# Kernel tuning notes

Measured on AMD Instinct MI355X. Metric: run time of the kernel, lower is better.

Reference implementation:

```python
import jax, jax.numpy as jnp
import numpy as np

BATCH = 8192
VOCAB = 16384
EMBED = 256
EPS = 1e-6


def setup_inputs() -> dict:
    key = jax.random.key(0)
    k1, k2 = jax.random.split(key)
    # multi-hot indicator input: values in {0,1}; only nonzero positions matter
    x = jax.random.randint(k1, (BATCH, VOCAB), 0, 2, dtype=jnp.int32)
    # learned embedding table (nn.Embedding weight)
    emb = jax.random.normal(k2, (VOCAB, EMBED), dtype=jnp.float32)
    return {"x": x, "emb": emb}


def reference(x, emb):
    # torch: gather embeddings at nonzero (row, col) pairs, scatter-add per row,
    # divide by per-row nonzero count (+eps). Equivalent jit-friendly form:
    # mask @ emb gives the per-row sum of embeddings over nonzero columns.
    mask = (x != 0).astype(emb.dtype)               # [B, V]
    embed_sum = mask @ emb                           # [B, E]
    count = jnp.sum(mask, axis=1, keepdims=True) + EPS  # [B, 1]
    return embed_sum / count
```

## Files before the change

### kernel.cpp

```cpp
#include <hip/hip_runtime.h>
#include <hip/hip_bf16.h>
#include <stdint.h>

#define BATCH 8192
#define VOCAB 16384
#define EMBED 256

#define BM 64
#define BK 64
#define KSPLIT 4
#define KRANGE (VOCAB / KSPLIT)
#define KITERS (KRANGE / BK)
#define MTILES (BATCH / BM)

typedef __attribute__((ext_vector_type(4))) float    f32x4;
typedef __attribute__((ext_vector_type(4))) int      i32x4;
typedef __attribute__((ext_vector_type(4))) unsigned u32x4;

#define EMB_WS_BYTES ((size_t)VOCAB * EMBED * 2)

__device__ __forceinline__ void gload_lds16(const void* g, void* l) {
    __builtin_amdgcn_global_load_lds(
        (const __attribute__((address_space(1))) unsigned int*)(uintptr_t)g,
        (__attribute__((address_space(3))) unsigned int*)(uint32_t)(uintptr_t)l,
        16, 0, 0);
}

__device__ __forceinline__ void mfma_bf16(f32x4& acc, i32x4 a, i32x4 b) {
    asm("v_mfma_f32_16x16x32_bf16 %0, %1, %2, %0" : "+v"(acc) : "v"(a), "v"(b));
}

__global__ __launch_bounds__(256) void prep_kernel(
    const float* __restrict__ emb, unsigned short* __restrict__ emb_ws,
    float* __restrict__ out)
{
    int t = blockIdx.x * 256 + threadIdx.x;
    ((f32x4*)out)[t] = (f32x4){0.f, 0.f, 0.f, 0.f};

    int ko = t >> 8;
    int e  = t & 255;
    union { unsigned short s[8]; u32x4 q; } v;
    #pragma unroll
    for (int j = 0; j < 8; ++j) {
        float f = emb[(size_t)(ko * 8 + j) * EMBED + e];
        unsigned u = __float_as_uint(f);
        u += 0x7FFFu + ((u >> 16) & 1u);
        v.s[j] = (unsigned short)(u >> 16);
    }
    int kt  = ko >> 3;
    int kk0 = (ko & 7) * 8;
    unsigned byt = (unsigned)(e * 128 + ((kk0 * 2) ^ ((e & 7) << 4)));
    *(u32x4*)((char*)emb_ws + (size_t)kt * 32768 + byt) = v.q;
}

__global__ __launch_bounds__(256) void gemm_kernel(
    const int* __restrict__ x, const unsigned short* __restrict__ emb_ws,
    float* __restrict__ out, int* __restrict__ cnt_ws)
{
    __shared__ __align__(16) unsigned short As[BM * BK];
    __shared__ __align__(16) unsigned short Bs[EMBED * BK];

    int bid   = blockIdx.x;
    int mt    = bid & (MTILES - 1);
    int split = bid >> 7;

    int tid  = threadIdx.x;
    int lane = tid & 63;
    int wave = tid >> 6;

    int ar = tid >> 2;
    int aq = tid & 3;
    const int*  aptr  = x + (size_t)(mt * BM + ar) * VOCAB + split * KRANGE + aq * 4;
    const char* bbase = (const char*)emb_ws + (size_t)split * KITERS * 32768;

    int cnt = 0;
    f32x4 acc[4][4];
    #pragma unroll
    for (int i = 0; i < 4; ++i)
        #pragma unroll
        for (int j = 0; j < 4; ++j) acc[i][j] = (f32x4){0.f, 0.f, 0.f, 0.f};

    for (int kt = 0; kt < KITERS; ++kt) {
        const char* bsrc = bbase + (size_t)kt * 32768 + tid * 16;
        #pragma unroll
        for (int i = 0; i < 8; ++i)
            gload_lds16(bsrc + i * 4096, (char*)Bs + tid * 16 + i * 4096);

        const int* ap = aptr + kt * BK;
        i32x4 av[4];
        #pragma unroll
        for (int j = 0; j < 4; ++j) av[j] = *(const i32x4*)(ap + j * 16);

        #pragma unroll
        for (int j = 0; j < 4; ++j) {
            unsigned lo = (av[j].x ? 0x3F80u : 0u) | (av[j].y ? 0x3F800000u : 0u);
            unsigned hi = (av[j].z ? 0x3F80u : 0u) | (av[j].w ? 0x3F800000u : 0u);
            cnt += (av[j].x != 0) + (av[j].y != 0) + (av[j].z != 0) + (av[j].w != 0);
            int kk = aq * 4 + j * 16;
            unsigned byt = (unsigned)(ar * 128 + ((kk * 2) ^ ((ar & 7) << 4)));
            *(uint2*)((char*)As + byt) = make_uint2(lo, hi);
        }

        __syncthreads();

        #pragma unroll
        for (int ks = 0; ks < 2; ++ks) {
            int kg = ks * 32 + (lane >> 4) * 8;
            i32x4 af[4], bf[4];
            #pragma unroll
            for (int fm = 0; fm < 4; ++fm) {
                int row = fm * 16 + (lane & 15);
                af[fm] = *(const i32x4*)((const char*)As + row * 128 +
                                         ((kg * 2) ^ ((row & 7) << 4)));
            }
            #pragma unroll
            for (int fe = 0; fe < 4; ++fe) {
                int e = wave * 64 + fe * 16 + (lane & 15);
                bf[fe] = *(const i32x4*)((const char*)Bs + e * 128 +
                                         ((kg * 2) ^ ((e & 7) << 4)));
            }
            #pragma unroll
            for (int fm = 0; fm < 4; ++fm)
                #pragma unroll
                for (int fe = 0; fe < 4; ++fe)
                    mfma_bf16(acc[fm][fe], af[fm], bf[fe]);
        }
        __syncthreads();
    }

    cnt += __shfl_xor(cnt, 1);
    cnt += __shfl_xor(cnt, 2);
    if (aq == 0) cnt_ws[split * BATCH + mt * BM + ar] = cnt;

    #pragma unroll
    for (int fm = 0; fm < 4; ++fm)
        #pragma unroll
        for (int fe = 0; fe < 4; ++fe)
            asm volatile("s_nop 7\n\ts_nop 7" : "+v"(acc[fm][fe]));

    #pragma unroll
    for (int fm = 0; fm < 4; ++fm) {
        int row = mt * BM + fm * 16 + (lane >> 4) * 4;
        #pragma unroll
        for (int fe = 0; fe < 4; ++fe) {
            int col = wave * 64 + fe * 16 + (lane & 15);
            float* p = out + (size_t)row * EMBED + col;
            #pragma unroll
            for (int r = 0; r < 4; ++r)
                atomicAdd(p + (size_t)r * EMBED, acc[fm][fe][r]);
        }
    }
}

__global__ __launch_bounds__(256) void div_kernel(
    float* __restrict__ out, const int* __restrict__ cnt_ws)
{
    int t = blockIdx.x * 256 + threadIdx.x;
    int b = t >> 6;
    float c = (float)(cnt_ws[b] + cnt_ws[BATCH + b] +
                      cnt_ws[2 * BATCH + b] + cnt_ws[3 * BATCH + b]);
    float inv = 1.0f / (c + 1e-6f);
    f32x4 v = ((f32x4*)out)[t];
    v.x *= inv; v.y *= inv; v.z *= inv; v.w *= inv;
    ((f32x4*)out)[t] = v;
}

extern "C" void kernel_launch(void* const* d_in, const int* in_sizes, int n_in,
                              void* d_out, int out_size, void* d_ws, size_t ws_size,
                              hipStream_t stream)
{
    const int*   x   = (const int*)d_in[0];
    const float* emb = (const float*)d_in[1];
    float*       out = (float*)d_out;

    unsigned short* emb_ws = (unsigned short*)d_ws;
    int*            cnt_ws = (int*)((char*)d_ws + EMB_WS_BYTES);

    prep_kernel<<<2048, 256, 0, stream>>>(emb, emb_ws, out);
    gemm_kernel<<<MTILES * KSPLIT, 256, 0, stream>>>(x, emb_ws, out, cnt_ws);
    div_kernel<<<2048, 256, 0, stream>>>(out, cnt_ws);
}
```

Baseline: 764.1 us.

## Replace atomic split-K reduction with partial buffers and raise split to eight

Doubles the K split to eight, giving 1024 blocks, and orders block IDs so the splits of one M tile run next to each other. Each block now writes its partial tile to its own workspace slice with plain stores instead of float atomics into the output. The divide kernel then sums the eight partials and the counts before normalising, so the output no longer needs zeroing in the prep kernel. This removes atomic contention and the zeroing pass. In exchange it writes and reads 64 MB of partial sums and needs a larger workspace.

```diff
diff --git a/kernel.cpp b/kernel.cpp
--- a/kernel.cpp
+++ b/kernel.cpp
@@ -8,7 +8,7 @@
 
 #define BM 64
 #define BK 64
-#define KSPLIT 4
+#define KSPLIT 8
 #define KRANGE (VOCAB / KSPLIT)
 #define KITERS (KRANGE / BK)
 #define MTILES (BATCH / BM)
@@ -18,6 +18,8 @@
 typedef __attribute__((ext_vector_type(4))) unsigned u32x4;
 
 #define EMB_WS_BYTES ((size_t)VOCAB * EMBED * 2)
+#define CNT_WS_BYTES ((size_t)KSPLIT * BATCH * 4)
+#define PART_STRIDE  ((size_t)BATCH * EMBED)
 
 __device__ __forceinline__ void gload_lds16(const void* g, void* l) {
     __builtin_amdgcn_global_load_lds(
@@ -31,12 +33,9 @@
 }
 
 __global__ __launch_bounds__(256) void prep_kernel(
-    const float* __restrict__ emb, unsigned short* __restrict__ emb_ws,
-    float* __restrict__ out)
+    const float* __restrict__ emb, unsigned short* __restrict__ emb_ws)
 {
     int t = blockIdx.x * 256 + threadIdx.x;
-    ((f32x4*)out)[t] = (f32x4){0.f, 0.f, 0.f, 0.f};
-
     int ko = t >> 8;
     int e  = t & 255;
     union { unsigned short s[8]; u32x4 q; } v;
@@ -53,16 +52,16 @@
     *(u32x4*)((char*)emb_ws + (size_t)kt * 32768 + byt) = v.q;
 }
 
-__global__ __launch_bounds__(256) void gemm_kernel(
+__global__ __launch_bounds__(256, 4) void gemm_kernel(
     const int* __restrict__ x, const unsigned short* __restrict__ emb_ws,
-    float* __restrict__ out, int* __restrict__ cnt_ws)
+    float* __restrict__ part_ws, int* __restrict__ cnt_ws)
 {
     __shared__ __align__(16) unsigned short As[BM * BK];
     __shared__ __align__(16) unsigned short Bs[EMBED * BK];
 
     int bid   = blockIdx.x;
-    int mt    = bid & (MTILES - 1);
-    int split = bid >> 7;
+    int split = bid & (KSPLIT - 1);
+    int mt    = bid >> 3;
 
     int tid  = threadIdx.x;
     int lane = tid & 63;
@@ -138,29 +137,37 @@
         for (int fe = 0; fe < 4; ++fe)
             asm volatile("s_nop 7\n\ts_nop 7" : "+v"(acc[fm][fe]));
 
+    float* part = part_ws + (size_t)split * PART_STRIDE;
     #pragma unroll
     for (int fm = 0; fm < 4; ++fm) {
         int row = mt * BM + fm * 16 + (lane >> 4) * 4;
         #pragma unroll
         for (int fe = 0; fe < 4; ++fe) {
             int col = wave * 64 + fe * 16 + (lane & 15);
-            float* p = out + (size_t)row * EMBED + col;
+            float* p = part + (size_t)row * EMBED + col;
             #pragma unroll
             for (int r = 0; r < 4; ++r)
-                atomicAdd(p + (size_t)r * EMBED, acc[fm][fe][r]);
+                p[(size_t)r * EMBED] = acc[fm][fe][r];
         }
     }
 }
 
 __global__ __launch_bounds__(256) void div_kernel(
-    float* __restrict__ out, const int* __restrict__ cnt_ws)
+    float* __restrict__ out, const float* __restrict__ part_ws,
+    const int* __restrict__ cnt_ws)
 {
     int t = blockIdx.x * 256 + threadIdx.x;
     int b = t >> 6;
-    float c = (float)(cnt_ws[b] + cnt_ws[BATCH + b] +
-                      cnt_ws[2 * BATCH + b] + cnt_ws[3 * BATCH + b]);
-    float inv = 1.0f / (c + 1e-6f);
-    f32x4 v = ((f32x4*)out)[t];
+    int c = 0;
+    #pragma unroll
+    for (int s = 0; s < KSPLIT; ++s) c += cnt_ws[s * BATCH + b];
+    float inv = 1.0f / ((float)c + 1e-6f);
+    f32x4 v = (f32x4){0.f, 0.f, 0.f, 0.f};
+    #pragma unroll
+    for (int s = 0; s < KSPLIT; ++s) {
+        f32x4 p = ((const f32x4*)(part_ws + s * PART_STRIDE))[t];
+        v.x += p.x; v.y += p.y; v.z += p.z; v.w += p.w;
+    }
     v.x *= inv; v.y *= inv; v.z *= inv; v.w *= inv;
     ((f32x4*)out)[t] = v;
 }
@@ -173,10 +180,11 @@
     const float* emb = (const float*)d_in[1];
     float*       out = (float*)d_out;
 
-    unsigned short* emb_ws = (unsigned short*)d_ws;
-    int*            cnt_ws = (int*)((char*)d_ws + EMB_WS_BYTES);
+    unsigned short* emb_ws  = (unsigned short*)d_ws;
+    int*            cnt_ws  = (int*)((char*)d_ws + EMB_WS_BYTES);
+    float*          part_ws = (float*)((char*)d_ws + EMB_WS_BYTES + CNT_WS_BYTES);
 
-    prep_kernel<<<2048, 256, 0, stream>>>(emb, emb_ws, out);
-    gemm_kernel<<<MTILES * KSPLIT, 256, 0, stream>>>(x, emb_ws, out, cnt_ws);
-    div_kernel<<<2048, 256, 0, stream>>>(out, cnt_ws);
+    prep_kernel<<<2048, 256, 0, stream>>>(emb, emb_ws);
+    gemm_kernel<<<MTILES * KSPLIT, 256, 0, stream>>>(x, emb_ws, part_ws, cnt_ws);
+    div_kernel<<<2048, 256, 0, stream>>>(out, part_ws, cnt_ws);
 }
```

Result: faster. 747.4 us (-2.2%).
